# Kernel tuning notes

Hardware: AMD Instinct MI355X
Metric: run time of the kernel (lower is better)

## Reference

```python
import jax, jax.numpy as jnp
import numpy as np

DIM = 1024
HEAD_DIM = 128
NUM_HEADS = 8
T = 8192
ATTN_SCALE = 0.1  # yarn.attn_scale after reset()
RMS_EPS = 1.1920929e-07  # torch F.rms_norm default eps for fp32


def setup_inputs() -> dict:
    key = jax.random.key(0)
    ks = jax.random.split(key, 6)
    x = jax.random.normal(ks[0], (1, T, DIM), jnp.float32)
    qkvo_w = jax.random.normal(ks[1], (4 * DIM, DIM), jnp.float32) * (DIM ** -0.5)
    ve = jax.random.normal(ks[2], (1, T, DIM), jnp.float32)
    sa_lambdas = jnp.array([0.9, 1.1], jnp.float32)
    attn_gate_w = jax.random.normal(ks[3], (NUM_HEADS, 12), jnp.float32) * 0.1
    ve_gate_w = jax.random.normal(ks[4], (NUM_HEADS, 12), jnp.float32) * 0.1
    # YaRN rotary factors, exactly as Yarn.reset()
    n_freq = HEAD_DIM // 4
    ang = (1.0 / 1024.0) ** jnp.linspace(0.0, 1.0, n_freq, dtype=jnp.float32)
    ang = jnp.repeat(ang, 2)                                   # [head_dim//2]
    ang = jnp.concatenate([ang, jnp.zeros(HEAD_DIM // 2, jnp.float32)])
    theta = jnp.arange(T, dtype=jnp.float32)[:, None] * ang[None, :]
    sign = jnp.where(jnp.arange(HEAD_DIM) % 2 == 1, -1.0, 1.0).astype(jnp.float32)
    factor1 = jnp.cos(theta)
    factor2 = jnp.sin(theta) * sign                            # odd lanes negated
    seqlens = jnp.array([0, 2048, 4096, 6144, 8192], jnp.int32)  # cu_seqlens
    return {"x": x, "qkvo_w": qkvo_w, "ve": ve, "sa_lambdas": sa_lambdas,
            "factor1": factor1, "factor2": factor2,
            "attn_gate_w": attn_gate_w, "ve_gate_w": ve_gate_w,
            "seqlens": seqlens, "bm_size": 128, "key_offset": 1}


def _rms_norm(x):
    return x * jax.lax.rsqrt(jnp.mean(x * x, axis=-1, keepdims=True) + RMS_EPS)


def _rotary(x, f1, f2):
    # x: [B, T, H, D]; pairwise flip of adjacent lanes, then f1*x + f2*flip(x)
    xf = x.reshape(*x.shape[:-1], x.shape[-1] // 2, 2)[..., ::-1].reshape(x.shape)
    return f1[None, :x.shape[1], None, :] * x + f2[None, :x.shape[1], None, :] * xf


def _windowed_varlen_attn(q, k, v, seqlens, bs, scale):
    # q,k,v: [T, H, D]; causal sliding window (bs left, 0 right), varlen via cu_seqlens.
    Tt, H, D = q.shape
    nb = Tt // bs
    pad = jnp.zeros((bs, H, D), q.dtype)
    kp = jnp.concatenate([pad, k], axis=0)
    vp = jnp.concatenate([pad, v], axis=0)
    idx = jnp.arange(nb)[:, None] * bs + jnp.arange(2 * bs)[None, :]   # [nb, 2bs] into padded
    kb, vb = kp[idx], vp[idx]                                          # [nb, 2bs, H, D]
    qb = q.reshape(nb, bs, H, D)
    gq = jnp.arange(Tt).reshape(nb, bs)                                # global query idx
    gk = idx - bs                                                      # global key idx (may be <0)
    seg = jnp.searchsorted(seqlens, jnp.arange(Tt), side='right')      # segment id per token
    sq = seg.reshape(nb, bs)
    sk = seg[jnp.clip(gk, 0, Tt - 1)]
    mask = ((gk[:, None, :] >= 0)
            & (gk[:, None, :] <= gq[:, :, None])
            & (gq[:, :, None] - gk[:, None, :] <= bs)
            & (sq[:, :, None] == sk[:, None, :]))                      # [nb, bs, 2bs]
    s = jnp.einsum('nqhd,nkhd->nhqk', qb, kb) * scale
    s = jnp.where(mask[:, None], s, -jnp.inf)
    p = jax.nn.softmax(s, axis=-1)
    return jnp.einsum('nhqk,nkhd->nqhd', p, vb).reshape(Tt, H, D)


def _forward(x, qkvo_w, ve, sa_lambdas, factor1, factor2, attn_gate_w, ve_gate_w,
             seqlens, bm_size, key_offset):
    B, Tt = x.shape[0], x.shape[1]
    H, D = NUM_HEADS, HEAD_DIM
    qkv = x @ (sa_lambdas[0] * qkvo_w[:3 * DIM]).T                    # [B, T, 3*dim]
    qkv = qkv.reshape(B, Tt, 3 * H, D)
    q, k, v = qkv[:, :, :H], qkv[:, :, H:2 * H], qkv[:, :, 2 * H:]
    q, k = _rms_norm(q), _rms_norm(k)
    q, k = _rotary(q, factor1, factor2), _rotary(k, factor1, factor2)
    if key_offset:
        hd2 = D // 2
        k_hi = jnp.concatenate([k[:, :1, :, hd2:], k[:, :-1, :, hd2:]], axis=1)
        k = jnp.concatenate([k[..., :hd2], k_hi], axis=-1)
    ve_gate = 2.0 * jax.nn.sigmoid(x[..., :12] @ ve_gate_w.T).reshape(B, Tt, H, 1)
    v = v + ve_gate * ve.reshape(B, Tt, H, D)
    y = _windowed_varlen_attn(q[0], k[0], v[0], seqlens, bm_size, ATTN_SCALE)
    y = y.reshape(B, Tt, H, D)
    y = y * jax.nn.sigmoid(x[..., :12] @ attn_gate_w.T).reshape(B, Tt, H, 1)
    y = y.reshape(B, Tt, H * D)
    return y @ (sa_lambdas[1] * qkvo_w[3 * DIM:]).T


def reference(x, qkvo_w, ve, sa_lambdas, factor1, factor2, attn_gate_w, ve_gate_w,
              seqlens, bm_size, key_offset):
    return _forward(x, qkvo_w, ve, sa_lambdas, factor1, factor2,
                    attn_gate_w, ve_gate_w, seqlens, bm_size, key_offset)
```

## Files before the change

### kernel.cpp

```cpp
#include <hip/hip_runtime.h>
#include <type_traits>


#define TSEQ 8192
#define DIMM 1024
#define NHEAD 8
#define HD 128
#define ATTN_SCALE 0.1f
#define RMS_EPS 1.1920929e-07f

typedef __bf16 bfx2 __attribute__((ext_vector_type(2)));
typedef __bf16 bfx4 __attribute__((ext_vector_type(4)));
typedef __bf16 bfx8 __attribute__((ext_vector_type(8)));
typedef float f32x4 __attribute__((ext_vector_type(4)));
typedef short s16x4 __attribute__((ext_vector_type(4)));

#define GLDS16(g, l)                                                         \
  __builtin_amdgcn_global_load_lds(                                          \
      (const __attribute__((address_space(1))) void*)(g),                    \
      (__attribute__((address_space(3))) void*)(l), 16, 0, 0)

__device__ __forceinline__ float sig_(float z) { return 1.0f / (1.0f + __expf(-z)); }

__global__ void k_prep(const float4* __restrict__ x, const float4* __restrict__ w,
                       const float* __restrict__ lam, bfx4* __restrict__ xb,
                       bfx4* __restrict__ w1b, bfx4* __restrict__ w2b) {
  const int nx = TSEQ * DIMM / 4;
  const int nw = 4096 * 1024 / 4;
  const float l0 = lam[0], l1 = lam[1];
  int i = blockIdx.x * blockDim.x + threadIdx.x;
  int stride = gridDim.x * blockDim.x;
  for (; i < nx + nw; i += stride) {
    if (i < nx) {
      float4 v = x[i];
      bfx4 o;
      o[0] = (__bf16)v.x; o[1] = (__bf16)v.y; o[2] = (__bf16)v.z; o[3] = (__bf16)v.w;
      xb[i] = o;
    } else {
      int j = i - nx;
      int row = (j * 4) >> 10;
      float s = (row < 3 * DIMM) ? l0 : l1;
      float4 v = w[j];
      bfx4 o;
      o[0] = (__bf16)(s * v.x); o[1] = (__bf16)(s * v.y);
      o[2] = (__bf16)(s * v.z); o[3] = (__bf16)(s * v.w);
      if (row < 3 * DIMM) w1b[j] = o;
      else                w2b[j - 3 * DIMM * DIMM / 4] = o;
    }
  }
}

template <typename CT>
__global__ __launch_bounds__(256, 2) void k_gemm2b(const __bf16* __restrict__ A,
                                                   const __bf16* __restrict__ B,
                                                   CT* __restrict__ C,
                                                   int M, int N, int K) {
  __shared__ __align__(16) __bf16 ldsb[2][256 * 64];
  const int tid = threadIdx.x;
  const int wave = tid >> 6, lane = tid & 63;
  const int wm = wave >> 1, wn = wave & 1;
  const int lr = lane & 15, lg = lane >> 4;
  const int bm = blockIdx.x, bn = blockIdx.y;

  const int srow = tid >> 3;
  const int scol = ((tid & 7) ^ (srow & 7)) * 8;
  const __bf16* Ag = A + (size_t)(bm * 128 + srow) * K + scol;
  const __bf16* Bg = B + (size_t)(bn * 128 + srow) * K + scol;

  char* buf0 = (char*)&ldsb[0][0];
  char* buf1 = (char*)&ldsb[1][0];

  auto stage = [&](int kt, char* buf) {
#pragma unroll
    for (int L = 0; L < 4; L++)
      GLDS16(Ag + (size_t)(L * 32) * K + kt * 64, buf + L * 4096 + wave * 1024);
#pragma unroll
    for (int L = 0; L < 4; L++)
      GLDS16(Bg + (size_t)(L * 32) * K + kt * 64, buf + 16384 + L * 4096 + wave * 1024);
  };

  const int aoffs = (wm * 64 + lr) * 128;
  const int boffs = 16384 + (wn * 64 + lr) * 128;
  const int s0 = (lg ^ (lr & 7)) * 16;
  const int s1 = ((4 + lg) ^ (lr & 7)) * 16;

  f32x4 acc[4][4] = {};

#define VMC0() asm volatile("s_waitcnt vmcnt(0)" ::: "memory")
#define BAR() __builtin_amdgcn_s_barrier()

  stage(0, buf0);
  VMC0(); BAR();

  const int NT = K / 64;
  for (int t = 0; t < NT; t++) {
    char* cur = (t & 1) ? buf1 : buf0;
    char* nxt = (t & 1) ? buf0 : buf1;
    if (t + 1 < NT) stage(t + 1, nxt);
    bfx8 af[4][2], bfr[4][2];
#pragma unroll
    for (int f = 0; f < 4; f++) {
      const char* p = cur + aoffs + f * 2048;
      af[f][0] = *(const bfx8*)(p + s0);
      af[f][1] = *(const bfx8*)(p + s1);
    }
#pragma unroll
    for (int f = 0; f < 4; f++) {
      const char* p = cur + boffs + f * 2048;
      bfr[f][0] = *(const bfx8*)(p + s0);
      bfr[f][1] = *(const bfx8*)(p + s1);
    }
    __builtin_amdgcn_s_setprio(1);
#pragma unroll
    for (int i = 0; i < 4; i++)
#pragma unroll
      for (int j = 0; j < 4; j++) {
        acc[i][j] = __builtin_amdgcn_mfma_f32_16x16x32_bf16(af[i][0], bfr[j][0], acc[i][j], 0, 0, 0);
        acc[i][j] = __builtin_amdgcn_mfma_f32_16x16x32_bf16(af[i][1], bfr[j][1], acc[i][j], 0, 0, 0);
      }
    __builtin_amdgcn_s_setprio(0);
    VMC0(); BAR();
  }

  const int rbase = bm * 128 + wm * 64 + lg * 4;
  const int cbase = bn * 128 + wn * 64 + lr;
#pragma unroll
  for (int f = 0; f < 4; f++)
#pragma unroll
    for (int rr = 0; rr < 4; rr++) {
      size_t rowoff = (size_t)(rbase + f * 16 + rr) * N + cbase;
#pragma unroll
      for (int nf = 0; nf < 4; nf++) C[rowoff + nf * 16] = (CT)acc[f][nf][rr];
    }
#undef VMC0
#undef BAR
}

template <int BM, typename CT>
__global__ __launch_bounds__(512, 2) void k_gemm8i(const __bf16* __restrict__ A,
                                                   const __bf16* __restrict__ B,
                                                   CT* __restrict__ C,
                                                   int M, int N, int K) {
  constexpr int MF = BM / 32, NF = 4;
  constexpr int MH = MF / 2;
  constexpr int LA = BM / 128, LB = 2;
  __shared__ __align__(16) __bf16 lds0s[(BM + 256) * 64];
  __shared__ __align__(16) __bf16 lds1s[(BM + 256) * 64];
  char* lds0 = (char*)lds0s;
  char* lds1 = (char*)lds1s;

  const int tid = threadIdx.x;
  const int wave = tid >> 6, lane = tid & 63;
  const int wm = wave >> 2, wn = wave & 3;
  const int lr = lane & 15, lg = lane >> 4;
  const int bm = blockIdx.x, bn = blockIdx.y;

  const int srow = tid >> 3;
  const int scol = ((tid & 7) ^ (srow & 7)) * 8;
  const __bf16* Ag = A + (size_t)(bm * BM + srow) * K + scol;
  const __bf16* Bg = B + (size_t)(bn * 256 + srow) * K + scol;

  auto stageAu = [&](int kt, int u, char* buf) {
#pragma unroll
    for (int L = 0; L < LA; L++)
      GLDS16(Ag + (size_t)(u * (BM / 2) + L * 64) * K + kt * 64,
             buf + (u * (BM / 2) + L * 64) * 128 + wave * 1024);
  };
  auto stageBu = [&](int kt, int u, char* buf) {
#pragma unroll
    for (int L = 0; L < LB; L++)
      GLDS16(Bg + (size_t)(u * 128 + L * 64) * K + kt * 64,
             buf + BM * 128 + (u * 128 + L * 64) * 128 + wave * 1024);
  };

  const int aoffs = (wm * (BM / 2) + lr) * 128;
  const int boffs = BM * 128 + (wn * 64 + lr) * 128;
  const int s0 = (lg ^ (lr & 7)) * 16;
  const int s1 = ((4 + lg) ^ (lr & 7)) * 16;

  f32x4 acc[MF][4] = {};
  bfx8 af[MH][2], bfr[4][2];

  auto readAf = [&](int i, const char* rbuf, int hf) {
    const char* p = rbuf + aoffs + (hf * MH + i) * 2048;
    af[i][0] = *(const bfx8*)(p + s0);
    af[i][1] = *(const bfx8*)(p + s1);
  };
  auto readBf = [&](int f, const char* rbuf) {
    const char* p = rbuf + boffs + f * 2048;
    bfr[f][0] = *(const bfx8*)(p + s0);
    bfr[f][1] = *(const bfx8*)(p + s1);
  };
  auto mfma2 = [&](int ha, int hb, int i, int j) {
    acc[ha * MH + i][hb * 2 + j] = __builtin_amdgcn_mfma_f32_16x16x32_bf16(
        af[i][0], bfr[hb * 2 + j][0], acc[ha * MH + i][hb * 2 + j], 0, 0, 0);
    acc[ha * MH + i][hb * 2 + j] = __builtin_amdgcn_mfma_f32_16x16x32_bf16(
        af[i][1], bfr[hb * 2 + j][1], acc[ha * MH + i][hb * 2 + j], 0, 0, 0);
  };
  auto clusterPlain = [&](int ha, int hb) {
    __builtin_amdgcn_s_setprio(1);
#pragma unroll
    for (int i = 0; i < MH; i++) { mfma2(ha, hb, i, 0); mfma2(ha, hb, i, 1); }
    __builtin_amdgcn_s_setprio(0);
  };
  auto clusterA_r = [&](int ha, int hb, const char* rbuf, int hf) {
    __builtin_amdgcn_s_setprio(1);
#pragma unroll
    for (int i = 0; i < MH; i++) {
      mfma2(ha, hb, i, 0); mfma2(ha, hb, i, 1);
      readAf(i, rbuf, hf);
      __builtin_amdgcn_sched_group_barrier(0x8, 4, 0);
      __builtin_amdgcn_sched_group_barrier(0x100, 2, 0);
    }
    __builtin_amdgcn_s_setprio(0);
  };
  auto clusterB_r = [&](int ha, int hb, const char* rbuf) {
    __builtin_amdgcn_s_setprio(1);
#pragma unroll
    for (int j = 0; j < 2; j++) {
#pragma unroll
      for (int i = 0; i < MH; i++) mfma2(ha, hb, i, j);
      readBf(hb * 2 + j, rbuf);
      __builtin_amdgcn_sched_group_barrier(0x8, MH * 2, 0);
      __builtin_amdgcn_sched_group_barrier(0x100, 2, 0);
    }
    __builtin_amdgcn_s_setprio(0);
  };

#define BAR() __builtin_amdgcn_s_barrier()
#define VMC(n) asm volatile("s_waitcnt vmcnt(%0)" ::"i"(n) : "memory")

  stageAu(0, 0, lds0); stageAu(0, 1, lds0);
  stageBu(0, 0, lds0); stageBu(0, 1, lds0);
  stageBu(1, 0, lds1); stageBu(1, 1, lds1);
  VMC(2 * LB); BAR();
#pragma unroll
  for (int i = 0; i < MH; i++) readAf(i, lds0, 0);
#pragma unroll
  for (int f = 0; f < 4; f++) readBf(f, lds0);

  int jj = 0;
  auto run_iter = [&](auto more_c) {
    constexpr bool more = decltype(more_c)::value;
    const int t1 = 2 * jj + 1, t2 = t1 + 1, t3 = t1 + 2;
    stageAu(t1, 0, lds1);
    clusterPlain(0, 0);
    BAR();
    stageAu(t1, 1, lds1);
    clusterA_r(0, 1, lds0, 1);
    VMC(2 * LA); BAR();
    if constexpr (more) stageBu(t2, 0, lds0);
    clusterB_r(1, 0, lds1);
    VMC(more ? LB : 0); BAR();
    if constexpr (more) stageBu(t2, 1, lds0);
    clusterA_r(1, 1, lds1, 0);
    readBf(2, lds1); readBf(3, lds1);
    BAR();
    if constexpr (more) stageAu(t2, 0, lds0);
    clusterPlain(0, 0);
    BAR();
    if constexpr (more) stageAu(t2, 1, lds0);
    clusterA_r(0, 1, lds1, 1);
    if constexpr (more) { VMC(2 * LA); }
    BAR();
    if constexpr (more) {
      stageBu(t3, 0, lds1);
      clusterB_r(1, 0, lds0);
      VMC(LB);
    } else {
      clusterPlain(1, 0);
    }
    BAR();
    if constexpr (more) {
      stageBu(t3, 1, lds1);
      clusterA_r(1, 1, lds0, 0);
      readBf(2, lds0); readBf(3, lds0);
    } else {
      clusterPlain(1, 1);
    }
    BAR();
    jj++;
  };

  const int NT2 = K / 128;
  for (int j = 0; j < NT2 - 1; j++) run_iter(std::integral_constant<bool, true>{});
  run_iter(std::integral_constant<bool, false>{});

  const int rbase = bm * BM + wm * (BM / 2) + lg * 4;
  const int cbase = bn * 256 + wn * 64 + lr;
#pragma unroll
  for (int f = 0; f < MF; f++)
#pragma unroll
    for (int rr = 0; rr < 4; rr++) {
      size_t rowoff = (size_t)(rbase + f * 16 + rr) * N + cbase;
#pragma unroll
      for (int nf = 0; nf < 4; nf++) C[rowoff + nf * 16] = (CT)acc[f][nf][rr];
    }
#undef BAR
#undef VMC
}

__global__ __launch_bounds__(512) void k_qk(
    const __bf16* __restrict__ qkv, const float* __restrict__ f1,
    const float* __restrict__ f2, const int* __restrict__ koff_p,
    __bf16* __restrict__ qb, __bf16* __restrict__ kb) {
  const int t = blockIdx.x;
  const int h = threadIdx.x >> 6;
  const int l = threadIdx.x & 63;
  const int d0 = 2 * l;
  const size_t qoff = (size_t)t * (3 * DIMM) + h * HD;

  bfx2 qv = *(const bfx2*)&qkv[qoff + d0];
  bfx2 kv = *(const bfx2*)&qkv[qoff + DIMM + d0];
  float q0 = (float)qv[0], q1 = (float)qv[1];
  float k0 = (float)kv[0], k1 = (float)kv[1];

  float sq = q0 * q0 + q1 * q1;
  float sk = k0 * k0 + k1 * k1;
#pragma unroll
  for (int off = 32; off; off >>= 1) {
    sq += __shfl_xor(sq, off);
    sk += __shfl_xor(sk, off);
  }
  float rq = rsqrtf(sq * (1.0f / 128.0f) + RMS_EPS);
  float rk = rsqrtf(sk * (1.0f / 128.0f) + RMS_EPS);
  q0 *= rq; q1 *= rq; k0 *= rk; k1 *= rk;

  float2 cc = *(const float2*)&f1[(size_t)t * HD + d0];
  float2 ss = *(const float2*)&f2[(size_t)t * HD + d0];
  float rq0 = cc.x * q0 + ss.x * q1, rq1 = cc.y * q1 + ss.y * q0;
  float rk0 = cc.x * k0 + ss.x * k1, rk1 = cc.y * k1 + ss.y * k0;

  bfx2 qo; qo[0] = (__bf16)rq0; qo[1] = (__bf16)rq1;
  *(bfx2*)&qb[(size_t)t * DIMM + h * HD + d0] = qo;

  bfx2 ko2; ko2[0] = (__bf16)rk0; ko2[1] = (__bf16)rk1;
  const int koff = *koff_p;
  const size_t kcol = (size_t)h * HD + d0;
  if (!koff || l < 32) {
    *(bfx2*)&kb[(size_t)t * DIMM + kcol] = ko2;
  } else {
    if (t + 1 < TSEQ) *(bfx2*)&kb[(size_t)(t + 1) * DIMM + kcol] = ko2;
    if (t == 0)       *(bfx2*)&kb[kcol] = ko2;
  }
}

__global__ __launch_bounds__(512) void k_vgate(
    const __bf16* __restrict__ qkv, const float* __restrict__ x,
    const float* __restrict__ ve, const float* __restrict__ agw,
    const float* __restrict__ vgw, __bf16* __restrict__ vT,
    float* __restrict__ ag) {
  __shared__ float vg_lds[64][4];
  __shared__ __bf16 vtile[HD][68];
  const int t0 = blockIdx.x * 64;
  const int hbase = blockIdx.y * 4;
  const int tid = threadIdx.x;

  if (tid < 256) {
    const int tl = tid >> 2, hh = tid & 3;
    const int h = hbase + hh;
    const int t = t0 + tl;
    float za = 0.0f, zg = 0.0f;
#pragma unroll
    for (int j = 0; j < 12; j++) {
      float xv = x[(size_t)t * DIMM + j];
      za += xv * agw[h * 12 + j];
      zg += xv * vgw[h * 12 + j];
    }
    ag[(size_t)t * NHEAD + h] = sig_(za);
    vg_lds[tl][hh] = 2.0f * sig_(zg);
  }
  __syncthreads();

  const int w = tid >> 6, l = tid & 63;
  const int dout = tid >> 2, tof = (tid & 3) * 16;
  for (int hh = 0; hh < 4; hh++) {
    const int h = hbase + hh;
#pragma unroll
    for (int it = 0; it < 8; it++) {
      const int tl = w * 8 + it;
      const int t = t0 + tl;
      const size_t voff = (size_t)t * (3 * DIMM) + 2 * DIMM + h * HD;
      float va = (float)qkv[voff + l];
      float vb = (float)qkv[voff + l + 64];
      float vea = ve[(size_t)t * DIMM + h * HD + l];
      float veb = ve[(size_t)t * DIMM + h * HD + l + 64];
      float gv = vg_lds[tl][hh];
      vtile[l][tl]      = (__bf16)(va + gv * vea);
      vtile[l + 64][tl] = (__bf16)(vb + gv * veb);
    }
    __syncthreads();
    {
      bfx4 a0 = *(const bfx4*)&vtile[dout][tof];
      bfx4 a1 = *(const bfx4*)&vtile[dout][tof + 4];
      bfx4 a2 = *(const bfx4*)&vtile[dout][tof + 8];
      bfx4 a3 = *(const bfx4*)&vtile[dout][tof + 12];
      bfx8 p0, p1;
      p0[0]=a0[0]; p0[1]=a0[1]; p0[2]=a0[2]; p0[3]=a0[3];
      p0[4]=a1[0]; p0[5]=a1[1]; p0[6]=a1[2]; p0[7]=a1[3];
      p1[0]=a2[0]; p1[1]=a2[1]; p1[2]=a2[2]; p1[3]=a2[3];
      p1[4]=a3[0]; p1[5]=a3[1]; p1[6]=a3[2]; p1[7]=a3[3];
      __bf16* dst = &vT[(size_t)(h * HD + dout) * TSEQ + t0 + tof];
      *(bfx8*)dst = p0;
      *(bfx8*)(dst + 8) = p1;
    }
    __syncthreads();
  }
}

__global__ __launch_bounds__(256, 4) void k_attn2(
    const __bf16* __restrict__ qb, const __bf16* __restrict__ kb,
    const __bf16* __restrict__ vT, const float* __restrict__ ag,
    const int* __restrict__ sl, int ns, __bf16* __restrict__ yb) {
  const int h = blockIdx.y;
  const int w = threadIdx.x >> 6, l = threadIdx.x & 63;
  const int lr = l & 15, lg = l >> 4;
  const int q0r = (blockIdx.x * 4 + w) * 16;
  const int kbase = q0r - 128;
  const int q = q0r + lr;
  const int kfs = (q0r < 128) ? ((128 - q0r) >> 4) : 0;

  bfx8 qf[4];
#pragma unroll
  for (int ds = 0; ds < 4; ds++)
    qf[ds] = *(const bfx8*)&qb[(size_t)q * DIMM + h * HD + ds * 32 + lg * 8];

  int segs = 0;
  for (int i = 0; i < ns; i++) {
    int v = sl[i];
    segs = (v <= q) ? ((v > segs) ? v : segs) : segs;
  }
  int klo = q - 128;
  if (segs > klo) klo = segs;
  if (klo < 0) klo = 0;

  f32x4 sf[9] = {};
#pragma unroll
  for (int kf = 0; kf < 9; kf++) {
    if (kf >= kfs) {
      const int krow = kbase + kf * 16 + lr;
      const __bf16* kp = &kb[(size_t)krow * DIMM + h * HD + lg * 8];
      bfx8 k0 = *(const bfx8*)(kp);
      bfx8 k1 = *(const bfx8*)(kp + 32);
      bfx8 k2 = *(const bfx8*)(kp + 64);
      bfx8 k3 = *(const bfx8*)(kp + 96);
      sf[kf] = __builtin_amdgcn_mfma_f32_16x16x32_bf16(k0, qf[0], sf[kf], 0, 0, 0);
      sf[kf] = __builtin_amdgcn_mfma_f32_16x16x32_bf16(k1, qf[1], sf[kf], 0, 0, 0);
      sf[kf] = __builtin_amdgcn_mfma_f32_16x16x32_bf16(k2, qf[2], sf[kf], 0, 0, 0);
      sf[kf] = __builtin_amdgcn_mfma_f32_16x16x32_bf16(k3, qf[3], sf[kf], 0, 0, 0);
    }
  }

#pragma unroll
  for (int kf = 0; kf < 9; kf++)
#pragma unroll
    for (int rr = 0; rr < 4; rr++) {
      int k = kbase + kf * 16 + lg * 4 + rr;
      bool valid = (k >= klo) && (k <= q);
      sf[kf][rr] = valid ? sf[kf][rr] * ATTN_SCALE : -1e30f;
    }

  float mx = -1e30f;
#pragma unroll
  for (int kf = 0; kf < 9; kf++)
#pragma unroll
    for (int rr = 0; rr < 4; rr++) mx = fmaxf(mx, sf[kf][rr]);
  mx = fmaxf(mx, __shfl_xor(mx, 16));
  mx = fmaxf(mx, __shfl_xor(mx, 32));

  float lsum = 0.0f;
#pragma unroll
  for (int kf = 0; kf < 9; kf++)
#pragma unroll
    for (int rr = 0; rr < 4; rr++) {
      float p = __expf(sf[kf][rr] - mx);
      sf[kf][rr] = p;
      lsum += p;
    }
  lsum += __shfl_xor(lsum, 16);
  lsum += __shfl_xor(lsum, 32);

  f32x4 o[8] = {};
#pragma unroll
  for (int kf = 0; kf < 9; kf++) {
    if (kf >= kfs) {
      bfx4 pc;
      pc[0] = (__bf16)sf[kf][0]; pc[1] = (__bf16)sf[kf][1];
      pc[2] = (__bf16)sf[kf][2]; pc[3] = (__bf16)sf[kf][3];
      s16x4 pb = *(s16x4*)&pc;
      const int kk = kbase + kf * 16 + 4 * lg;
#pragma unroll
      for (int nf = 0; nf < 8; nf++) {
        s16x4 vf = *(const s16x4*)&vT[(size_t)(h * HD + nf * 16 + lr) * TSEQ + kk];
        o[nf] = __builtin_amdgcn_mfma_f32_16x16x16bf16_1k(vf, pb, o[nf], 0, 0, 0);
      }
    }
  }

  const float sc = ag[(size_t)q * NHEAD + h] / lsum;
#pragma unroll
  for (int nf = 0; nf < 8; nf++) {
    bfx4 st;
#pragma unroll
    for (int rr = 0; rr < 4; rr++) st[rr] = (__bf16)(o[nf][rr] * sc);
    *(bfx4*)&yb[(size_t)q * DIMM + h * HD + nf * 16 + lg * 4] = st;
  }
}

extern "C" void kernel_launch(void* const* d_in, const int* in_sizes, int n_in,
                              void* d_out, int out_size, void* d_ws, size_t ws_size,
                              hipStream_t stream) {
  const float* x   = (const float*)d_in[0];
  const float* qw  = (const float*)d_in[1];
  const float* ve  = (const float*)d_in[2];
  const float* lam = (const float*)d_in[3];
  const float* f1  = (const float*)d_in[4];
  const float* f2  = (const float*)d_in[5];
  const float* agw = (const float*)d_in[6];
  const float* vgw = (const float*)d_in[7];
  const int*   sl  = (const int*)d_in[8];
  const int    ns  = in_sizes[8];
  const int*   koff = (const int*)d_in[10];
  float* out = (float*)d_out;
  char* ws = (char*)d_ws;

  const size_t MB = 1024 * 1024;
  if (ws_size < 105 * MB) return;
  __bf16* xb   = (__bf16*)(ws);
  __bf16* w1b  = (__bf16*)(ws + 16 * MB);
  __bf16* w2b  = (__bf16*)(ws + 22 * MB);
  __bf16* qkvb = (__bf16*)(ws + 24 * MB);
  __bf16* qbuf = (__bf16*)(ws + 72 * MB);
  __bf16* kbuf = (__bf16*)(ws + 88 * MB);
  float*  ag   = (float*)(ws + 104 * MB);
  __bf16* vT   = xb;
  __bf16* ybuf = qkvb;

  k_prep<<<3072, 256, 0, stream>>>((const float4*)x, (const float4*)qw, lam,
                                   (bfx4*)xb, (bfx4*)w1b, (bfx4*)w2b);
  k_gemm2b<__bf16><<<dim3(TSEQ / 128, 3 * DIMM / 128), 256, 0, stream>>>(
      xb, w1b, qkvb, TSEQ, 3 * DIMM, DIMM);
  k_qk<<<TSEQ, 512, 0, stream>>>(qkvb, f1, f2, koff, qbuf, kbuf);
  k_vgate<<<dim3(TSEQ / 64, 2), 512, 0, stream>>>(qkvb, x, ve, agw, vgw, vT, ag);
  k_attn2<<<dim3(TSEQ / 64, NHEAD), 256, 0, stream>>>(qbuf, kbuf, vT, ag, sl, ns, ybuf);
  k_gemm8i<128, float><<<dim3(TSEQ / 128, DIMM / 256), 512, 0, stream>>>(
      ybuf, w2b, out, TSEQ, DIMM, DIMM);
}
```

Before: 171.2 us.

## Stage shared K and V windows in LDS per 128-query block in attention

Reworks the windowed attention kernel so each 512-thread block handles 128 queries of one head. The block loads the 256-row K window and matching V^T tile into swizzled LDS using direct global-to-LDS loads, and every wave then reads its K and V fragments from LDS. The goal is to stop each 16-query wave from refetching the overlapping K and V rows from global memory. The cost is 128KB of LDS per block, so only one block fits per CU, with less latency hiding and a full barrier before any compute starts.

```diff
diff --git a/kernel.cpp b/kernel.cpp
--- a/kernel.cpp
+++ b/kernel.cpp
@@ -408,15 +408,19 @@
   }
 }
 
-__global__ __launch_bounds__(256, 4) void k_attn2(
+__global__ __launch_bounds__(512, 1) void k_attn3(
     const __bf16* __restrict__ qb, const __bf16* __restrict__ kb,
     const __bf16* __restrict__ vT, const float* __restrict__ ag,
     const int* __restrict__ sl, int ns, __bf16* __restrict__ yb) {
-  const int h = blockIdx.y;
-  const int w = threadIdx.x >> 6, l = threadIdx.x & 63;
+  __shared__ __align__(16) char kls[65536];
+  __shared__ __align__(16) char vls[65536];
+  const int n = blockIdx.x, h = blockIdx.y;
+  const int tid = threadIdx.x;
+  const int w = tid >> 6, l = tid & 63;
   const int lr = l & 15, lg = l >> 4;
-  const int q0r = (blockIdx.x * 4 + w) * 16;
+  const int q0r = n * 128 + w * 16;
   const int kbase = q0r - 128;
+  const int kbb = n * 128 - 128;
   const int q = q0r + lr;
   const int kfs = (q0r < 128) ? ((128 - q0r) >> 4) : 0;
 
@@ -424,6 +428,32 @@
 #pragma unroll
   for (int ds = 0; ds < 4; ds++)
     qf[ds] = *(const bfx8*)&qb[(size_t)q * DIMM + h * HD + ds * 32 + lg * 8];
+
+  {
+    const int rr_ = tid >> 4;
+    const int slot = tid & 15;
+#pragma unroll
+    for (int r = 0; r < 8; r++) {
+      const int rel = r * 32 + rr_;
+      int grow = kbb + rel;
+      grow = grow < 0 ? 0 : grow;
+      const int slotp = slot ^ (rel & 15);
+      GLDS16(kb + (size_t)grow * DIMM + h * HD + slotp * 8,
+             kls + r * 8192 + w * 1024);
+    }
+  }
+  {
+    const int slot = l & 31;
+#pragma unroll
+    for (int r = 0; r < 8; r++) {
+      const int d = r * 16 + w * 2 + (l >> 5);
+      const int slotp = slot ^ (d & 15);
+      int tsrc = kbb + slotp * 8;
+      tsrc = tsrc < 0 ? 0 : tsrc;
+      GLDS16(vT + (size_t)(h * HD + d) * TSEQ + tsrc,
+             vls + r * 8192 + w * 1024);
+    }
+  }
 
   int segs = 0;
   for (int i = 0; i < ns; i++) {
@@ -434,16 +464,20 @@
   if (segs > klo) klo = segs;
   if (klo < 0) klo = 0;
 
+  asm volatile("s_waitcnt vmcnt(0)" ::: "memory");
+  __builtin_amdgcn_s_barrier();
+
+  const int kswz = lr << 4;
   f32x4 sf[9] = {};
 #pragma unroll
   for (int kf = 0; kf < 9; kf++) {
     if (kf >= kfs) {
-      const int krow = kbase + kf * 16 + lr;
-      const __bf16* kp = &kb[(size_t)krow * DIMM + h * HD + lg * 8];
-      bfx8 k0 = *(const bfx8*)(kp);
-      bfx8 k1 = *(const bfx8*)(kp + 32);
-      bfx8 k2 = *(const bfx8*)(kp + 64);
-      bfx8 k3 = *(const bfx8*)(kp + 96);
+      const int relrow = w * 16 + kf * 16 + lr;
+      const char* kp = kls + relrow * 256;
+      bfx8 k0 = *(const bfx8*)(kp + ((lg * 16) ^ kswz));
+      bfx8 k1 = *(const bfx8*)(kp + ((64 + lg * 16) ^ kswz));
+      bfx8 k2 = *(const bfx8*)(kp + ((128 + lg * 16) ^ kswz));
+      bfx8 k3 = *(const bfx8*)(kp + ((192 + lg * 16) ^ kswz));
       sf[kf] = __builtin_amdgcn_mfma_f32_16x16x32_bf16(k0, qf[0], sf[kf], 0, 0, 0);
       sf[kf] = __builtin_amdgcn_mfma_f32_16x16x32_bf16(k1, qf[1], sf[kf], 0, 0, 0);
       sf[kf] = __builtin_amdgcn_mfma_f32_16x16x32_bf16(k2, qf[2], sf[kf], 0, 0, 0);
@@ -488,10 +522,10 @@
       pc[0] = (__bf16)sf[kf][0]; pc[1] = (__bf16)sf[kf][1];
       pc[2] = (__bf16)sf[kf][2]; pc[3] = (__bf16)sf[kf][3];
       s16x4 pb = *(s16x4*)&pc;
-      const int kk = kbase + kf * 16 + 4 * lg;
+      const int tof = (w * 32 + kf * 32 + lg * 8) ^ kswz;
 #pragma unroll
       for (int nf = 0; nf < 8; nf++) {
-        s16x4 vf = *(const s16x4*)&vT[(size_t)(h * HD + nf * 16 + lr) * TSEQ + kk];
+        s16x4 vf = *(const s16x4*)(vls + (nf * 16 + lr) * 512 + tof);
         o[nf] = __builtin_amdgcn_mfma_f32_16x16x16bf16_1k(vf, pb, o[nf], 0, 0, 0);
       }
     }
@@ -542,7 +576,7 @@
       xb, w1b, qkvb, TSEQ, 3 * DIMM, DIMM);
   k_qk<<<TSEQ, 512, 0, stream>>>(qkvb, f1, f2, koff, qbuf, kbuf);
   k_vgate<<<dim3(TSEQ / 64, 2), 512, 0, stream>>>(qkvb, x, ve, agw, vgw, vT, ag);
-  k_attn2<<<dim3(TSEQ / 64, NHEAD), 256, 0, stream>>>(qbuf, kbuf, vT, ag, sl, ns, ybuf);
+  k_attn3<<<dim3(TSEQ / 128, NHEAD), 512, 0, stream>>>(qbuf, kbuf, vT, ag, sl, ns, ybuf);
   k_gemm8i<128, float><<<dim3(TSEQ / 128, DIMM / 256), 512, 0, stream>>>(
       ybuf, w2b, out, TSEQ, DIMM, DIMM);
 }
```

Result: faster. 143.5 us (-16.2%).
